# Performance work log

Hardware: AMD Instinct MI355X
Metric: run time of the kernel (lower is better)

Reference implementation:

```python
import jax, jax.numpy as jnp
import numpy as np

N_FULL, N_SUB, NNZ = 100000, 32768, 1048576
F_IN, DH, DOUT = 512, 512, 512
EPS_NORM = 1e-9   # HighOrderAggregator 'norm' bias eps
EPS_L2 = 1e-12    # F.normalize eps


def spmm(row, col, val, feat, n):
    # sparse [n,n] @ dense [n,d] via gather + segment-sum scatter
    return jax.ops.segment_sum(val[:, None] * feat[col], row, num_segments=n)


def ho_layer(row, col, val, feat, Ws, bs, scales, offsets, n):
    # HighOrderAggregator, order=1, act=relu, bias='norm', aggr='concat'
    hops = [feat, spmm(row, col, val, feat, n)]
    parts = []
    for h, W, b, s, o in zip(hops, Ws, bs, scales, offsets):
        f = jax.nn.relu(h @ W.T + b)
        mean = jnp.mean(f, axis=1, keepdims=True)
        var = jnp.var(f, axis=1, keepdims=True)  # unbiased=False, matches torch
        parts.append((f - mean) * s * jax.lax.rsqrt(var + EPS_NORM) + o)
    return jnp.concatenate(parts, axis=1)


def _xavier(k, shape):
    fan_out, fan_in = shape
    lim = float(np.sqrt(6.0 / (fan_in + fan_out)))
    return jax.random.uniform(k, shape, jnp.float32, -lim, lim)


def setup_inputs() -> dict:
    key = jax.random.key(0)
    ks = jax.random.split(key, 24)
    inp = {}
    inp['feat_full'] = jax.random.normal(ks[0], (N_FULL, F_IN), jnp.float32)
    inp['node_subgraph'] = jax.random.randint(ks[1], (N_SUB,), 0, N_FULL)
    inp['adj_row'] = jax.random.randint(ks[2], (NNZ,), 0, N_SUB)
    inp['adj_col'] = jax.random.randint(ks[3], (NNZ,), 0, N_SUB)
    inp['adj_val'] = jax.random.uniform(ks[4], (NNZ,), jnp.float32)
    # layer 1: dim_in=512 -> 512 per order, concat -> 1024
    inp['W1_0'] = _xavier(ks[5], (DH, F_IN))
    inp['W1_1'] = _xavier(ks[6], (DH, F_IN))
    inp['b1_0'] = 0.02 * jax.random.normal(ks[7], (DH,), jnp.float32)
    inp['b1_1'] = 0.02 * jax.random.normal(ks[8], (DH,), jnp.float32)
    inp['s1_0'] = 1.0 + 0.1 * jax.random.normal(ks[9], (DH,), jnp.float32)
    inp['s1_1'] = 1.0 + 0.1 * jax.random.normal(ks[10], (DH,), jnp.float32)
    inp['o1_0'] = 0.02 * jax.random.normal(ks[11], (DH,), jnp.float32)
    inp['o1_1'] = 0.02 * jax.random.normal(ks[12], (DH,), jnp.float32)
    # layer 2: dim_in=1024 -> 512 per order, concat -> 1024
    inp['W2_0'] = _xavier(ks[13], (DH, 2 * DH))
    inp['W2_1'] = _xavier(ks[14], (DH, 2 * DH))
    inp['b2_0'] = 0.02 * jax.random.normal(ks[15], (DH,), jnp.float32)
    inp['b2_1'] = 0.02 * jax.random.normal(ks[16], (DH,), jnp.float32)
    inp['s2_0'] = 1.0 + 0.1 * jax.random.normal(ks[17], (DH,), jnp.float32)
    inp['s2_1'] = 1.0 + 0.1 * jax.random.normal(ks[18], (DH,), jnp.float32)
    inp['o2_0'] = 0.02 * jax.random.normal(ks[19], (DH,), jnp.float32)
    inp['o2_1'] = 0.02 * jax.random.normal(ks[20], (DH,), jnp.float32)
    # classifier: order=0, act='I', bias='bias'
    inp['Wc'] = _xavier(ks[21], (DOUT, 2 * DH))
    inp['bc'] = 0.02 * jax.random.normal(ks[22], (DOUT,), jnp.float32)
    return inp


def reference(feat_full, node_subgraph, adj_row, adj_col, adj_val,
              W1_0, W1_1, b1_0, b1_1, s1_0, s1_1, o1_0, o1_1,
              W2_0, W2_1, b2_0, b2_1, s2_0, s2_1, o2_0, o2_1,
              Wc, bc):
    feat = feat_full[node_subgraph]                       # [N_SUB, F_IN] gather
    h = ho_layer(adj_row, adj_col, adj_val, feat,
                 (W1_0, W1_1), (b1_0, b1_1), (s1_0, s1_1), (o1_0, o1_1), N_SUB)
    h = ho_layer(adj_row, adj_col, adj_val, h,
                 (W2_0, W2_1), (b2_0, b2_1), (s2_0, s2_1), (o2_0, o2_1), N_SUB)
    nrm = jnp.linalg.norm(h, axis=1, keepdims=True)       # F.normalize p=2 dim=1
    h = h / jnp.maximum(nrm, EPS_L2)
    return h @ Wc.T + bc                                  # classifier (act='I')
```

## Files before the change

kernel.cpp:

```cpp
#include <hip/hip_runtime.h>
#include <stdint.h>

typedef unsigned short u16;
typedef unsigned int u32;

#define NSUB 32768
#define NNZ_E 1048576

using short8 = __attribute__((ext_vector_type(8))) short;
using f32x4  = __attribute__((ext_vector_type(4))) float;

__device__ __forceinline__ u16 f2b(float f) {
  u32 u = __float_as_uint(f);
  return (u16)((u + 0x7fffu + ((u >> 16) & 1u)) >> 16);
}
__device__ __forceinline__ float b2f(u16 x) {
  return __uint_as_float(((u32)x) << 16);
}

__device__ __forceinline__ void glds16(const void* g, void* l) {
  __builtin_amdgcn_global_load_lds(
      (const __attribute__((address_space(1))) u32*)g,
      (__attribute__((address_space(3))) u32*)l, 16, 0, 0);
}

__global__ __launch_bounds__(256) void cvt_bf16(const float* __restrict__ in,
                                                u16* __restrict__ out, int n4) {
  int i = blockIdx.x * 256 + threadIdx.x;
  if (i < n4) {
    float4 v = ((const float4*)in)[i];
    ushort4 o;
    o.x = f2b(v.x); o.y = f2b(v.y); o.z = f2b(v.z); o.w = f2b(v.w);
    ((ushort4*)out)[i] = o;
  }
}

__global__ __launch_bounds__(128) void gather_cast(const float* __restrict__ ff,
                                                   const int* __restrict__ idx,
                                                   u16* __restrict__ out) {
  int r = blockIdx.x, t = threadIdx.x;
  size_t src = (size_t)idx[r];
  float4 v = *(const float4*)(ff + src * 512 + t * 4);
  ushort4 o;
  o.x = f2b(v.x); o.y = f2b(v.y); o.z = f2b(v.z); o.w = f2b(v.w);
  *(ushort4*)(out + (size_t)r * 512 + t * 4) = o;
}

__global__ __launch_bounds__(256) void edge_count(const int* __restrict__ row,
                                                  int* __restrict__ cnt) {
  int i = blockIdx.x * 256 + threadIdx.x;
  atomicAdd(&cnt[row[i]], 1);
}

__global__ __launch_bounds__(1024) void scan_rows(const int* __restrict__ cnt,
                                                  int* __restrict__ off,
                                                  int* __restrict__ cursor) {
  __shared__ int part[1024];
  int t = threadIdx.x;
  int base = t * 32;
  int sum = 0;
  for (int j = 0; j < 32; ++j) sum += cnt[base + j];
  part[t] = sum;
  __syncthreads();
  for (int d = 1; d < 1024; d <<= 1) {
    int v = part[t];
    int u = (t >= d) ? part[t - d] : 0;
    __syncthreads();
    part[t] = v + u;
    __syncthreads();
  }
  int run = part[t] - sum;
  for (int j = 0; j < 32; ++j) {
    int c = cnt[base + j];
    off[base + j] = run;
    cursor[base + j] = run;
    run += c;
  }
  if (t == 1023) off[NSUB] = part[1023];
}

__global__ __launch_bounds__(256) void edge_scatter(const int* __restrict__ row,
                                                    const int* __restrict__ col,
                                                    const float* __restrict__ val,
                                                    int* __restrict__ cursor,
                                                    int2* __restrict__ cv) {
  int i = blockIdx.x * 256 + threadIdx.x;
  int r = row[i];
  int p = atomicAdd(&cursor[r], 1);
  int2 e; e.x = col[i]; e.y = __float_as_int(val[i]);
  cv[p] = e;
}

__device__ __forceinline__ void fma8(int4 u, float v, float* a) {
  u32 w;
  w = (u32)u.x; a[0] += v * __uint_as_float(w << 16); a[1] += v * __uint_as_float(w & 0xffff0000u);
  w = (u32)u.y; a[2] += v * __uint_as_float(w << 16); a[3] += v * __uint_as_float(w & 0xffff0000u);
  w = (u32)u.z; a[4] += v * __uint_as_float(w << 16); a[5] += v * __uint_as_float(w & 0xffff0000u);
  w = (u32)u.w; a[6] += v * __uint_as_float(w << 16); a[7] += v * __uint_as_float(w & 0xffff0000u);
}

template <int LDX, bool NORM>
__global__ __launch_bounds__(256) void spmm512(const int* __restrict__ off,
                                               const int2* __restrict__ cv,
                                               const u16* __restrict__ X,
                                               u16* __restrict__ Y, int ldy,
                                               const float* __restrict__ bias,
                                               const float* __restrict__ sc,
                                               const float* __restrict__ ofs) {
  const int lane = threadIdx.x & 63, wave = threadIdx.x >> 6;
  const int r = blockIdx.x * 4 + wave;
  const int s = __builtin_amdgcn_readfirstlane(off[r]);
  const int e = __builtin_amdgcn_readfirstlane(off[r + 1]);
  float a[8] = {0.f, 0.f, 0.f, 0.f, 0.f, 0.f, 0.f, 0.f};
  const u16* Xl = X + lane * 8;
  int i = s;
  for (; i + 4 <= e; i += 4) {
    int2 p0 = cv[i], p1 = cv[i + 1], p2 = cv[i + 2], p3 = cv[i + 3];
    int4 u0 = *(const int4*)(Xl + (size_t)p0.x * LDX);
    int4 u1 = *(const int4*)(Xl + (size_t)p1.x * LDX);
    int4 u2 = *(const int4*)(Xl + (size_t)p2.x * LDX);
    int4 u3 = *(const int4*)(Xl + (size_t)p3.x * LDX);
    fma8(u0, __int_as_float(p0.y), a);
    fma8(u1, __int_as_float(p1.y), a);
    fma8(u2, __int_as_float(p2.y), a);
    fma8(u3, __int_as_float(p3.y), a);
  }
  for (; i < e; ++i) {
    int2 p0 = cv[i];
    int4 u0 = *(const int4*)(Xl + (size_t)p0.x * LDX);
    fma8(u0, __int_as_float(p0.y), a);
  }
  if (NORM) {
    float4 b0 = *(const float4*)(bias + lane * 8);
    float4 b1 = *(const float4*)(bias + lane * 8 + 4);
    a[0] = fmaxf(a[0] + b0.x, 0.f); a[1] = fmaxf(a[1] + b0.y, 0.f);
    a[2] = fmaxf(a[2] + b0.z, 0.f); a[3] = fmaxf(a[3] + b0.w, 0.f);
    a[4] = fmaxf(a[4] + b1.x, 0.f); a[5] = fmaxf(a[5] + b1.y, 0.f);
    a[6] = fmaxf(a[6] + b1.z, 0.f); a[7] = fmaxf(a[7] + b1.w, 0.f);
    float sum = 0.f, sq = 0.f;
#pragma unroll
    for (int j = 0; j < 8; ++j) { sum += a[j]; sq += a[j] * a[j]; }
#pragma unroll
    for (int d = 1; d < 64; d <<= 1) {
      sum += __shfl_xor(sum, d);
      sq  += __shfl_xor(sq, d);
    }
    float mean = sum * (1.f / 512.f);
    float var = sq * (1.f / 512.f) - mean * mean;
    float rstd = rsqrtf(var + 1e-9f);
    float4 s0 = *(const float4*)(sc + lane * 8);
    float4 s1 = *(const float4*)(sc + lane * 8 + 4);
    float4 o0 = *(const float4*)(ofs + lane * 8);
    float4 o1 = *(const float4*)(ofs + lane * 8 + 4);
    int4 o;
    o.x = (int)((u32)f2b((a[0] - mean) * s0.x * rstd + o0.x) |
                ((u32)f2b((a[1] - mean) * s0.y * rstd + o0.y) << 16));
    o.y = (int)((u32)f2b((a[2] - mean) * s0.z * rstd + o0.z) |
                ((u32)f2b((a[3] - mean) * s0.w * rstd + o0.w) << 16));
    o.z = (int)((u32)f2b((a[4] - mean) * s1.x * rstd + o1.x) |
                ((u32)f2b((a[5] - mean) * s1.y * rstd + o1.y) << 16));
    o.w = (int)((u32)f2b((a[6] - mean) * s1.z * rstd + o1.z) |
                ((u32)f2b((a[7] - mean) * s1.w * rstd + o1.w) << 16));
    *(int4*)(Y + (size_t)r * ldy + lane * 8) = o;
  } else {
    int4 o;
    o.x = (int)((u32)f2b(a[0]) | ((u32)f2b(a[1]) << 16));
    o.y = (int)((u32)f2b(a[2]) | ((u32)f2b(a[3]) << 16));
    o.z = (int)((u32)f2b(a[4]) | ((u32)f2b(a[5]) << 16));
    o.w = (int)((u32)f2b(a[6]) | ((u32)f2b(a[7]) << 16));
    *(int4*)(Y + (size_t)r * ldy + lane * 8) = o;
  }
}

template <int K, int LDC, bool BIAS, bool BF16OUT>
__global__ __launch_bounds__(256) void gemm_bt(const u16* __restrict__ A,
                                               const u16* __restrict__ W,
                                               const float* __restrict__ bias,
                                               float* __restrict__ Cf,
                                               u16* __restrict__ Cb) {
  __shared__ __align__(16) u16 As[128 * 32];
  __shared__ __align__(16) u16 Bs[128 * 32];
  const int t = threadIdx.x;
  const int lane = t & 63, wave = t >> 6;
  const int wm = (wave >> 1) * 64, wn = (wave & 1) * 64;
  const int nwg = gridDim.x * gridDim.y;
  const int bid = blockIdx.x + gridDim.x * blockIdx.y;
  const int sbid = (bid % 8) * (nwg / 8) + bid / 8;
  const int bx = sbid % gridDim.x, by = sbid / gridDim.x;
  const int m0 = by * 128, n0 = bx * 128;

  f32x4 acc[4][4];
#pragma unroll
  for (int m = 0; m < 4; ++m)
#pragma unroll
    for (int n = 0; n < 4; ++n) acc[m][n] = f32x4{0.f, 0.f, 0.f, 0.f};

  const int lr = t >> 2;
  const int lc = (t & 3) * 8;
  const u16* Ag  = A + (size_t)(m0 + lr) * K + lc;
  const u16* Ag2 = Ag + (size_t)64 * K;
  const u16* Wg  = W + (size_t)(n0 + lr) * K + lc;
  const u16* Wg2 = Wg + (size_t)64 * K;
  char* asb0 = (char*)As + wave * 1024;
  char* asb1 = (char*)As + 4096 + wave * 1024;
  char* bsb0 = (char*)Bs + wave * 1024;
  char* bsb1 = (char*)Bs + 4096 + wave * 1024;
  const int fr = lane & 15, kh = lane >> 4;

  for (int kt = 0; kt < K / 32; ++kt) {
    glds16(Ag + kt * 32, asb0);
    glds16(Ag2 + kt * 32, asb1);
    glds16(Wg + kt * 32, bsb0);
    glds16(Wg2 + kt * 32, bsb1);
    __syncthreads();
    short8 af[4], bfr[4];
#pragma unroll
    for (int m = 0; m < 4; ++m)
      af[m] = *(const short8*)&As[(wm + m * 16 + fr) * 32 + kh * 8];
#pragma unroll
    for (int n = 0; n < 4; ++n)
      bfr[n] = *(const short8*)&Bs[(wn + n * 16 + fr) * 32 + kh * 8];
#pragma unroll
    for (int m = 0; m < 4; ++m)
#pragma unroll
      for (int n = 0; n < 4; ++n)
        acc[m][n] = __builtin_amdgcn_mfma_f32_16x16x32_bf16(af[m], bfr[n], acc[m][n], 0, 0, 0);
    __syncthreads();
  }

  const int crow = (lane >> 4) * 4;
  const int ccol = lane & 15;
#pragma unroll
  for (int n = 0; n < 4; ++n) {
    int col = n0 + wn + n * 16 + ccol;
    float bv = BIAS ? bias[col] : 0.f;
#pragma unroll
    for (int m = 0; m < 4; ++m) {
      int row = m0 + wm + m * 16 + crow;
#pragma unroll
      for (int q = 0; q < 4; ++q) {
        float v = acc[m][n][q] + bv;
        if (BF16OUT)
          Cb[(size_t)(row + q) * LDC + col] = f2b(v);
        else
          Cf[(size_t)(row + q) * LDC + col] = v;
      }
    }
  }
}

__global__ __launch_bounds__(128) void rownorm_b(const u16* __restrict__ F, int ldf,
                                                 const float* __restrict__ bias,
                                                 const float* __restrict__ sc,
                                                 const float* __restrict__ ofs,
                                                 u16* __restrict__ out, int col_off) {
  int r = blockIdx.x, t = threadIdx.x;
  ushort4 uv = *(const ushort4*)(F + (size_t)r * ldf + t * 4);
  float4 b4 = *(const float4*)(bias + t * 4);
  float4 v;
  v.x = fmaxf(b2f(uv.x) + b4.x, 0.f);
  v.y = fmaxf(b2f(uv.y) + b4.y, 0.f);
  v.z = fmaxf(b2f(uv.z) + b4.z, 0.f);
  v.w = fmaxf(b2f(uv.w) + b4.w, 0.f);
  float sum = v.x + v.y + v.z + v.w;
  float sq = v.x * v.x + v.y * v.y + v.z * v.z + v.w * v.w;
  for (int d = 32; d > 0; d >>= 1) {
    sum += __shfl_down(sum, d);
    sq  += __shfl_down(sq, d);
  }
  __shared__ float red[4];
  if ((t & 63) == 0) { red[(t >> 6) * 2] = sum; red[(t >> 6) * 2 + 1] = sq; }
  __syncthreads();
  float S = red[0] + red[2], Q = red[1] + red[3];
  float mean = S * (1.f / 512.f);
  float var = Q * (1.f / 512.f) - mean * mean;
  float rstd = rsqrtf(var + 1e-9f);
  float4 s4 = *(const float4*)(sc + t * 4);
  float4 o4 = *(const float4*)(ofs + t * 4);
  ushort4 o;
  o.x = f2b((v.x - mean) * s4.x * rstd + o4.x);
  o.y = f2b((v.y - mean) * s4.y * rstd + o4.y);
  o.z = f2b((v.z - mean) * s4.z * rstd + o4.z);
  o.w = f2b((v.w - mean) * s4.w * rstd + o4.w);
  *(ushort4*)(out + (size_t)r * 1024 + col_off + t * 4) = o;
}

__global__ __launch_bounds__(256) void l2norm(u16* __restrict__ H) {
  int r = blockIdx.x, t = threadIdx.x;
  uint2 u = *(const uint2*)(H + (size_t)r * 1024 + t * 4);
  float f0 = __uint_as_float(u.x << 16);
  float f1 = __uint_as_float(u.x & 0xffff0000u);
  float f2 = __uint_as_float(u.y << 16);
  float f3 = __uint_as_float(u.y & 0xffff0000u);
  float sq = f0 * f0 + f1 * f1 + f2 * f2 + f3 * f3;
  for (int d = 32; d > 0; d >>= 1) sq += __shfl_down(sq, d);
  __shared__ float red[4];
  if ((t & 63) == 0) red[t >> 6] = sq;
  __syncthreads();
  float S = red[0] + red[1] + red[2] + red[3];
  float inv = 1.f / fmaxf(sqrtf(S), 1e-12f);
  uint2 o;
  o.x = (u32)f2b(f0 * inv) | ((u32)f2b(f1 * inv) << 16);
  o.y = (u32)f2b(f2 * inv) | ((u32)f2b(f3 * inv) << 16);
  *(uint2*)(H + (size_t)r * 1024 + t * 4) = o;
}

extern "C" void kernel_launch(void* const* d_in, const int* in_sizes, int n_in,
                              void* d_out, int out_size, void* d_ws, size_t ws_size,
                              hipStream_t stream) {
  (void)in_sizes; (void)n_in; (void)out_size; (void)ws_size;
  const float* feat_full = (const float*)d_in[0];
  const int*   nodes = (const int*)d_in[1];
  const int*   arow = (const int*)d_in[2];
  const int*   acol = (const int*)d_in[3];
  const float* aval = (const float*)d_in[4];
  const float* W1_0 = (const float*)d_in[5];
  const float* W1_1 = (const float*)d_in[6];
  const float* b1_0 = (const float*)d_in[7];
  const float* b1_1 = (const float*)d_in[8];
  const float* s1_0 = (const float*)d_in[9];
  const float* s1_1 = (const float*)d_in[10];
  const float* o1_0 = (const float*)d_in[11];
  const float* o1_1 = (const float*)d_in[12];
  const float* W2_0 = (const float*)d_in[13];
  const float* W2_1 = (const float*)d_in[14];
  const float* b2_0 = (const float*)d_in[15];
  const float* b2_1 = (const float*)d_in[16];
  const float* s2_0 = (const float*)d_in[17];
  const float* s2_1 = (const float*)d_in[18];
  const float* o2_0 = (const float*)d_in[19];
  const float* o2_1 = (const float*)d_in[20];
  const float* Wc = (const float*)d_in[21];
  const float* bc = (const float*)d_in[22];
  float* out = (float*)d_out;

  const size_t MB = (size_t)1 << 20;
  char* p = (char*)d_ws;
  u16* FEAT = (u16*)p;
  u16* S1   = (u16*)(p + 32 * MB);
  u16* H1   = (u16*)(p + 64 * MB);
  u16* H2   = (u16*)(p + 128 * MB);
  u16* TMPb = (u16*)(p + 192 * MB);
  u16* TTL  = (u16*)(p + 192 * MB);
  u16* W1_0b = (u16*)(p + 256 * MB);
  u16* W1_1b = W1_0b + 512 * 512;
  u16* W2cat = W1_1b + 512 * 512;
  u16* Wcb   = W2cat + 1024 * 1024;
  int* row_off = (int*)(p + 264 * MB);
  int* cnt    = row_off + 33024;
  int* cursor = cnt + NSUB;
  int2* cv    = (int2*)(cursor + NSUB);

  hipMemsetAsync(cnt, 0, NSUB * sizeof(int), stream);

  cvt_bf16<<<(512 * 512 / 4 + 255) / 256, 256, 0, stream>>>(W1_0, W1_0b, 512 * 512 / 4);
  cvt_bf16<<<(512 * 512 / 4 + 255) / 256, 256, 0, stream>>>(W1_1, W1_1b, 512 * 512 / 4);
  cvt_bf16<<<(512 * 1024 / 4 + 255) / 256, 256, 0, stream>>>(W2_0, W2cat, 512 * 1024 / 4);
  cvt_bf16<<<(512 * 1024 / 4 + 255) / 256, 256, 0, stream>>>(W2_1, W2cat + 512 * 1024, 512 * 1024 / 4);
  cvt_bf16<<<(512 * 1024 / 4 + 255) / 256, 256, 0, stream>>>(Wc, Wcb, 512 * 1024 / 4);

  gather_cast<<<NSUB, 128, 0, stream>>>(feat_full, nodes, FEAT);

  edge_count<<<NNZ_E / 256, 256, 0, stream>>>(arow, cnt);
  scan_rows<<<1, 1024, 0, stream>>>(cnt, row_off, cursor);
  edge_scatter<<<NNZ_E / 256, 256, 0, stream>>>(arow, acol, aval, cursor, cv);

  spmm512<512, false><<<NSUB / 4, 256, 0, stream>>>(row_off, cv, FEAT, S1, 512,
                                                    nullptr, nullptr, nullptr);
  gemm_bt<512, 512, false, true><<<dim3(4, 256), 256, 0, stream>>>(FEAT, W1_0b, nullptr, nullptr, TMPb);
  rownorm_b<<<NSUB, 128, 0, stream>>>(TMPb, 512, b1_0, s1_0, o1_0, H1, 0);
  gemm_bt<512, 512, false, true><<<dim3(4, 256), 256, 0, stream>>>(S1, W1_1b, nullptr, nullptr, TMPb);
  rownorm_b<<<NSUB, 128, 0, stream>>>(TMPb, 512, b1_1, s1_1, o1_1, H1, 512);

  gemm_bt<1024, 1024, false, true><<<dim3(8, 256), 256, 0, stream>>>(H1, W2cat, nullptr, nullptr, TTL);
  rownorm_b<<<NSUB, 128, 0, stream>>>(TTL, 1024, b2_0, s2_0, o2_0, H2, 0);
  spmm512<1024, true><<<NSUB / 4, 256, 0, stream>>>(row_off, cv, TTL + 512, H2 + 512, 1024,
                                                    b2_1, s2_1, o2_1);

  l2norm<<<NSUB, 256, 0, stream>>>(H2);
  gemm_bt<1024, 512, true, false><<<dim3(4, 256), 256, 0, stream>>>(H2, Wcb, bc, out, nullptr);
}
```

Measured before the change: 725.3 us.

## Fuse GEMM with bias-ReLU-rownorm epilogue and fold L2 norm into classifier

Adds a gemm_norm kernel in which each 512-thread block computes full 512-wide output rows for 64 rows. Bias, ReLU, mean/variance and the affine norm are applied in the epilogue, so the separate rownorm passes and their bf16 intermediate buffers are no longer needed. The L2 normalize no longer rewrites H2; a light kernel computes per-row inverse norms, and the classifier GEMM scales its accumulator by them. The trade is a 64-row tile that reloads the full weight slab per block, which lowers weight reuse and may lower MFMA efficiency compared with the 128x128 tiles.

```diff
diff --git a/kernel.cpp b/kernel.cpp
--- a/kernel.cpp
+++ b/kernel.cpp
@@ -172,10 +172,128 @@
   }
 }
 
-template <int K, int LDC, bool BIAS, bool BF16OUT>
+template <int K>
+__global__ __launch_bounds__(512) void gemm_norm(const u16* __restrict__ A,
+                                                 const u16* __restrict__ W,
+                                                 const float* __restrict__ bias,
+                                                 const float* __restrict__ sc,
+                                                 const float* __restrict__ ofs,
+                                                 u16* __restrict__ out, int col_off) {
+  __shared__ __align__(16) u16 As[64 * 32];
+  __shared__ __align__(16) u16 Bs[512 * 32];
+  __shared__ float redS[8][64];
+  __shared__ float redQ[8][64];
+  __shared__ float mrs[2][64];
+  const int t = threadIdx.x;
+  const int lane = t & 63, w = t >> 6;
+  const int wn = w * 64;
+  const int m0 = blockIdx.x * 64;
+  const int fr = lane & 15, kh = lane >> 4;
+
+  f32x4 acc[4][4];
+#pragma unroll
+  for (int m = 0; m < 4; ++m)
+#pragma unroll
+    for (int n = 0; n < 4; ++n) acc[m][n] = f32x4{0.f, 0.f, 0.f, 0.f};
+
+  const int kc8 = (lane & 3) * 8;
+  const u16* Ag = A + (size_t)(m0 + w * 16 + (lane >> 2)) * K + kc8;
+  const u16* Wg = W + (size_t)(w * 64 + (lane >> 2)) * K + kc8;
+  char* asb = (char*)As + w * 1024;
+  char* bsb = (char*)Bs + w * 4096;
+
+  for (int kt = 0; kt < K / 32; ++kt) {
+    if (w < 4) glds16(Ag + kt * 32, asb);
+    glds16(Wg + kt * 32, bsb);
+    glds16(Wg + (size_t)16 * K + kt * 32, bsb + 1024);
+    glds16(Wg + (size_t)32 * K + kt * 32, bsb + 2048);
+    glds16(Wg + (size_t)48 * K + kt * 32, bsb + 3072);
+    __syncthreads();
+    short8 af[4], bfr[4];
+#pragma unroll
+    for (int m = 0; m < 4; ++m)
+      af[m] = *(const short8*)&As[(m * 16 + fr) * 32 + kh * 8];
+#pragma unroll
+    for (int n = 0; n < 4; ++n)
+      bfr[n] = *(const short8*)&Bs[(wn + n * 16 + fr) * 32 + kh * 8];
+#pragma unroll
+    for (int m = 0; m < 4; ++m)
+#pragma unroll
+      for (int n = 0; n < 4; ++n)
+        acc[m][n] = __builtin_amdgcn_mfma_f32_16x16x32_bf16(af[m], bfr[n], acc[m][n], 0, 0, 0);
+    __syncthreads();
+  }
+
+  float bv[4], sv[4], ov[4];
+#pragma unroll
+  for (int n = 0; n < 4; ++n) {
+    int cg = wn + n * 16 + fr;
+    bv[n] = bias[cg]; sv[n] = sc[cg]; ov[n] = ofs[cg];
+  }
+  float s_[4][4], q_[4][4];
+#pragma unroll
+  for (int m = 0; m < 4; ++m)
+#pragma unroll
+    for (int q = 0; q < 4; ++q) { s_[m][q] = 0.f; q_[m][q] = 0.f; }
+#pragma unroll
+  for (int m = 0; m < 4; ++m)
+#pragma unroll
+    for (int n = 0; n < 4; ++n)
+#pragma unroll
+      for (int q = 0; q < 4; ++q) {
+        float v = fmaxf(acc[m][n][q] + bv[n], 0.f);
+        acc[m][n][q] = v;
+        s_[m][q] += v; q_[m][q] += v * v;
+      }
+#pragma unroll
+  for (int d = 1; d < 16; d <<= 1)
+#pragma unroll
+    for (int m = 0; m < 4; ++m)
+#pragma unroll
+      for (int q = 0; q < 4; ++q) {
+        s_[m][q] += __shfl_xor(s_[m][q], d);
+        q_[m][q] += __shfl_xor(q_[m][q], d);
+      }
+  if (fr == 0) {
+#pragma unroll
+    for (int m = 0; m < 4; ++m)
+#pragma unroll
+      for (int q = 0; q < 4; ++q) {
+        int row = m * 16 + kh * 4 + q;
+        redS[w][row] = s_[m][q];
+        redQ[w][row] = q_[m][q];
+      }
+  }
+  __syncthreads();
+  if (t < 64) {
+    float S = 0.f, Q = 0.f;
+#pragma unroll
+    for (int w8 = 0; w8 < 8; ++w8) { S += redS[w8][t]; Q += redQ[w8][t]; }
+    float mean = S * (1.f / 512.f);
+    float var = Q * (1.f / 512.f) - mean * mean;
+    mrs[0][t] = mean;
+    mrs[1][t] = rsqrtf(var + 1e-9f);
+  }
+  __syncthreads();
+#pragma unroll
+  for (int m = 0; m < 4; ++m)
+#pragma unroll
+    for (int q = 0; q < 4; ++q) {
+      int row = m * 16 + kh * 4 + q;
+      float mean = mrs[0][row], rstd = mrs[1][row];
+#pragma unroll
+      for (int n = 0; n < 4; ++n) {
+        float v = (acc[m][n][q] - mean) * sv[n] * rstd + ov[n];
+        out[(size_t)(m0 + row) * 1024 + col_off + wn + n * 16 + fr] = f2b(v);
+      }
+    }
+}
+
+template <int K, int LDC, bool BIAS, bool BF16OUT, bool RS>
 __global__ __launch_bounds__(256) void gemm_bt(const u16* __restrict__ A,
                                                const u16* __restrict__ W,
                                                const float* __restrict__ bias,
+                                               const float* __restrict__ rs,
                                                float* __restrict__ Cf,
                                                u16* __restrict__ Cb) {
   __shared__ __align__(16) u16 As[128 * 32];
@@ -239,7 +357,9 @@
       int row = m0 + wm + m * 16 + crow;
 #pragma unroll
       for (int q = 0; q < 4; ++q) {
-        float v = acc[m][n][q] + bv;
+        float v = acc[m][n][q];
+        if (RS) v *= rs[row + q];
+        v += bv;
         if (BF16OUT)
           Cb[(size_t)(row + q) * LDC + col] = f2b(v);
         else
@@ -249,60 +369,25 @@
   }
 }
 
-__global__ __launch_bounds__(128) void rownorm_b(const u16* __restrict__ F, int ldf,
-                                                 const float* __restrict__ bias,
-                                                 const float* __restrict__ sc,
-                                                 const float* __restrict__ ofs,
-                                                 u16* __restrict__ out, int col_off) {
-  int r = blockIdx.x, t = threadIdx.x;
-  ushort4 uv = *(const ushort4*)(F + (size_t)r * ldf + t * 4);
-  float4 b4 = *(const float4*)(bias + t * 4);
-  float4 v;
-  v.x = fmaxf(b2f(uv.x) + b4.x, 0.f);
-  v.y = fmaxf(b2f(uv.y) + b4.y, 0.f);
-  v.z = fmaxf(b2f(uv.z) + b4.z, 0.f);
-  v.w = fmaxf(b2f(uv.w) + b4.w, 0.f);
-  float sum = v.x + v.y + v.z + v.w;
-  float sq = v.x * v.x + v.y * v.y + v.z * v.z + v.w * v.w;
-  for (int d = 32; d > 0; d >>= 1) {
-    sum += __shfl_down(sum, d);
-    sq  += __shfl_down(sq, d);
-  }
-  __shared__ float red[4];
-  if ((t & 63) == 0) { red[(t >> 6) * 2] = sum; red[(t >> 6) * 2 + 1] = sq; }
-  __syncthreads();
-  float S = red[0] + red[2], Q = red[1] + red[3];
-  float mean = S * (1.f / 512.f);
-  float var = Q * (1.f / 512.f) - mean * mean;
-  float rstd = rsqrtf(var + 1e-9f);
-  float4 s4 = *(const float4*)(sc + t * 4);
-  float4 o4 = *(const float4*)(ofs + t * 4);
-  ushort4 o;
-  o.x = f2b((v.x - mean) * s4.x * rstd + o4.x);
-  o.y = f2b((v.y - mean) * s4.y * rstd + o4.y);
-  o.z = f2b((v.z - mean) * s4.z * rstd + o4.z);
-  o.w = f2b((v.w - mean) * s4.w * rstd + o4.w);
-  *(ushort4*)(out + (size_t)r * 1024 + col_off + t * 4) = o;
-}
-
-__global__ __launch_bounds__(256) void l2norm(u16* __restrict__ H) {
-  int r = blockIdx.x, t = threadIdx.x;
-  uint2 u = *(const uint2*)(H + (size_t)r * 1024 + t * 4);
-  float f0 = __uint_as_float(u.x << 16);
-  float f1 = __uint_as_float(u.x & 0xffff0000u);
-  float f2 = __uint_as_float(u.y << 16);
-  float f3 = __uint_as_float(u.y & 0xffff0000u);
-  float sq = f0 * f0 + f1 * f1 + f2 * f2 + f3 * f3;
-  for (int d = 32; d > 0; d >>= 1) sq += __shfl_down(sq, d);
-  __shared__ float red[4];
-  if ((t & 63) == 0) red[t >> 6] = sq;
-  __syncthreads();
-  float S = red[0] + red[1] + red[2] + red[3];
-  float inv = 1.f / fmaxf(sqrtf(S), 1e-12f);
-  uint2 o;
-  o.x = (u32)f2b(f0 * inv) | ((u32)f2b(f1 * inv) << 16);
-  o.y = (u32)f2b(f2 * inv) | ((u32)f2b(f3 * inv) << 16);
-  *(uint2*)(H + (size_t)r * 1024 + t * 4) = o;
+__global__ __launch_bounds__(256) void l2scale(const u16* __restrict__ H,
+                                               float* __restrict__ rn) {
+  const int lane = threadIdx.x & 63, wave = threadIdx.x >> 6;
+  const int r = blockIdx.x * 4 + wave;
+  const u16* row = H + (size_t)r * 1024 + lane * 16;
+  int4 u0 = *(const int4*)row;
+  int4 u1 = *(const int4*)(row + 8);
+  float sq = 0.f;
+  const int vals[8] = {u0.x, u0.y, u0.z, u0.w, u1.x, u1.y, u1.z, u1.w};
+#pragma unroll
+  for (int j = 0; j < 8; ++j) {
+    u32 wv = (u32)vals[j];
+    float f0 = __uint_as_float(wv << 16);
+    float f1 = __uint_as_float(wv & 0xffff0000u);
+    sq += f0 * f0 + f1 * f1;
+  }
+#pragma unroll
+  for (int d = 1; d < 64; d <<= 1) sq += __shfl_xor(sq, d);
+  if (lane == 0) rn[r] = 1.f / fmaxf(sqrtf(sq), 1e-12f);
 }
 
 extern "C" void kernel_launch(void* const* d_in, const int* in_sizes, int n_in,
@@ -340,12 +425,13 @@
   u16* S1   = (u16*)(p + 32 * MB);
   u16* H1   = (u16*)(p + 64 * MB);
   u16* H2   = (u16*)(p + 128 * MB);
-  u16* TMPb = (u16*)(p + 192 * MB);
-  u16* TTL  = (u16*)(p + 192 * MB);
+  u16* G2   = (u16*)(p + 192 * MB);
+  float* RN = (float*)(p + 224 * MB);
   u16* W1_0b = (u16*)(p + 256 * MB);
   u16* W1_1b = W1_0b + 512 * 512;
-  u16* W2cat = W1_1b + 512 * 512;
-  u16* Wcb   = W2cat + 1024 * 1024;
+  u16* W2_0b = W1_1b + 512 * 512;
+  u16* W2_1b = W2_0b + 512 * 1024;
+  u16* Wcb   = W2_1b + 512 * 1024;
   int* row_off = (int*)(p + 264 * MB);
   int* cnt    = row_off + 33024;
   int* cursor = cnt + NSUB;
@@ -355,8 +441,8 @@
 
   cvt_bf16<<<(512 * 512 / 4 + 255) / 256, 256, 0, stream>>>(W1_0, W1_0b, 512 * 512 / 4);
   cvt_bf16<<<(512 * 512 / 4 + 255) / 256, 256, 0, stream>>>(W1_1, W1_1b, 512 * 512 / 4);
-  cvt_bf16<<<(512 * 1024 / 4 + 255) / 256, 256, 0, stream>>>(W2_0, W2cat, 512 * 1024 / 4);
-  cvt_bf16<<<(512 * 1024 / 4 + 255) / 256, 256, 0, stream>>>(W2_1, W2cat + 512 * 1024, 512 * 1024 / 4);
+  cvt_bf16<<<(512 * 1024 / 4 + 255) / 256, 256, 0, stream>>>(W2_0, W2_0b, 512 * 1024 / 4);
+  cvt_bf16<<<(512 * 1024 / 4 + 255) / 256, 256, 0, stream>>>(W2_1, W2_1b, 512 * 1024 / 4);
   cvt_bf16<<<(512 * 1024 / 4 + 255) / 256, 256, 0, stream>>>(Wc, Wcb, 512 * 1024 / 4);
 
   gather_cast<<<NSUB, 128, 0, stream>>>(feat_full, nodes, FEAT);
@@ -367,16 +453,16 @@
 
   spmm512<512, false><<<NSUB / 4, 256, 0, stream>>>(row_off, cv, FEAT, S1, 512,
                                                     nullptr, nullptr, nullptr);
-  gemm_bt<512, 512, false, true><<<dim3(4, 256), 256, 0, stream>>>(FEAT, W1_0b, nullptr, nullptr, TMPb);
-  rownorm_b<<<NSUB, 128, 0, stream>>>(TMPb, 512, b1_0, s1_0, o1_0, H1, 0);
-  gemm_bt<512, 512, false, true><<<dim3(4, 256), 256, 0, stream>>>(S1, W1_1b, nullptr, nullptr, TMPb);
-  rownorm_b<<<NSUB, 128, 0, stream>>>(TMPb, 512, b1_1, s1_1, o1_1, H1, 512);
-
-  gemm_bt<1024, 1024, false, true><<<dim3(8, 256), 256, 0, stream>>>(H1, W2cat, nullptr, nullptr, TTL);
-  rownorm_b<<<NSUB, 128, 0, stream>>>(TTL, 1024, b2_0, s2_0, o2_0, H2, 0);
-  spmm512<1024, true><<<NSUB / 4, 256, 0, stream>>>(row_off, cv, TTL + 512, H2 + 512, 1024,
-                                                    b2_1, s2_1, o2_1);
-
-  l2norm<<<NSUB, 256, 0, stream>>>(H2);
-  gemm_bt<1024, 512, true, false><<<dim3(4, 256), 256, 0, stream>>>(H2, Wcb, bc, out, nullptr);
-}
+  gemm_norm<512><<<NSUB / 64, 512, 0, stream>>>(FEAT, W1_0b, b1_0, s1_0, o1_0, H1, 0);
+  gemm_norm<512><<<NSUB / 64, 512, 0, stream>>>(S1, W1_1b, b1_1, s1_1, o1_1, H1, 512);
+
+  gemm_norm<1024><<<NSUB / 64, 512, 0, stream>>>(H1, W2_0b, b2_0, s2_0, o2_0, H2, 0);
+  gemm_bt<1024, 512, false, true, false><<<dim3(4, 256), 256, 0, stream>>>(
+      H1, W2_1b, nullptr, nullptr, nullptr, G2);
+  spmm512<512, true><<<NSUB / 4, 256, 0, stream>>>(row_off, cv, G2, H2 + 512, 1024,
+                                                   b2_1, s2_1, o2_1);
+
+  l2scale<<<NSUB / 4, 256, 0, stream>>>(H2, RN);
+  gemm_bt<1024, 512, true, false, true><<<dim3(4, 256), 256, 0, stream>>>(
+      H2, Wcb, bc, RN, out, nullptr);
+}
```

Result: slower. 768.0 us (+5.9%).

## Bucket CSR edges by column block; fold L2 norm into classifier GEMM epilogue

Applied to the files above, without the earlier changes.

Edges within each row are now grouped into 8 column buckets (col>>12), so SpMM gathers within a row hit nearby X rows, which is meant to improve cache locality. The count and scan work grows eightfold to 262144 counters, all scanned by a single block. The L2 normalization no longer rewrites H2 in place. A per-row inverse norm is computed instead and applied as a row scale in the classifier GEMM epilogue, saving one read-write pass over H2 in exchange for a slightly different rounding order (no bf16 rounding of the normalized values).

```diff
diff --git a/kernel.cpp b/kernel.cpp
--- a/kernel.cpp
+++ b/kernel.cpp
@@ -46,20 +46,21 @@
   *(ushort4*)(out + (size_t)r * 512 + t * 4) = o;
 }
 
-__global__ __launch_bounds__(256) void edge_count(const int* __restrict__ row,
-                                                  int* __restrict__ cnt) {
+__global__ __launch_bounds__(256) void edge_count8(const int* __restrict__ row,
+                                                   const int* __restrict__ col,
+                                                   int* __restrict__ cnt8) {
   int i = blockIdx.x * 256 + threadIdx.x;
-  atomicAdd(&cnt[row[i]], 1);
-}
-
-__global__ __launch_bounds__(1024) void scan_rows(const int* __restrict__ cnt,
-                                                  int* __restrict__ off,
-                                                  int* __restrict__ cursor) {
+  atomicAdd(&cnt8[row[i] * 8 + (col[i] >> 12)], 1);
+}
+
+__global__ __launch_bounds__(1024) void scan_rows8(const int* __restrict__ cnt8,
+                                                   int* __restrict__ off,
+                                                   int* __restrict__ cursor8) {
   __shared__ int part[1024];
   int t = threadIdx.x;
-  int base = t * 32;
+  int base = t * 256;
   int sum = 0;
-  for (int j = 0; j < 32; ++j) sum += cnt[base + j];
+  for (int j = 0; j < 256; ++j) sum += cnt8[base + j];
   part[t] = sum;
   __syncthreads();
   for (int d = 1; d < 1024; d <<= 1) {
@@ -70,24 +71,25 @@
     __syncthreads();
   }
   int run = part[t] - sum;
-  for (int j = 0; j < 32; ++j) {
-    int c = cnt[base + j];
-    off[base + j] = run;
-    cursor[base + j] = run;
+  for (int j = 0; j < 256; ++j) {
+    int idx = base + j;
+    int c = cnt8[idx];
+    cursor8[idx] = run;
+    if ((idx & 7) == 0) off[idx >> 3] = run;
     run += c;
   }
-  if (t == 1023) off[NSUB] = part[1023];
-}
-
-__global__ __launch_bounds__(256) void edge_scatter(const int* __restrict__ row,
-                                                    const int* __restrict__ col,
-                                                    const float* __restrict__ val,
-                                                    int* __restrict__ cursor,
-                                                    int2* __restrict__ cv) {
+  if (t == 1023) off[NSUB] = run;
+}
+
+__global__ __launch_bounds__(256) void edge_scatter8(const int* __restrict__ row,
+                                                     const int* __restrict__ col,
+                                                     const float* __restrict__ val,
+                                                     int* __restrict__ cursor8,
+                                                     int2* __restrict__ cv) {
   int i = blockIdx.x * 256 + threadIdx.x;
-  int r = row[i];
-  int p = atomicAdd(&cursor[r], 1);
-  int2 e; e.x = col[i]; e.y = __float_as_int(val[i]);
+  int c = col[i];
+  int p = atomicAdd(&cursor8[row[i] * 8 + (c >> 12)], 1);
+  int2 e; e.x = c; e.y = __float_as_int(val[i]);
   cv[p] = e;
 }
 
@@ -172,10 +174,11 @@
   }
 }
 
-template <int K, int LDC, bool BIAS, bool BF16OUT>
+template <int K, int LDC, bool BIAS, bool BF16OUT, bool RS>
 __global__ __launch_bounds__(256) void gemm_bt(const u16* __restrict__ A,
                                                const u16* __restrict__ W,
                                                const float* __restrict__ bias,
+                                               const float* __restrict__ rs,
                                                float* __restrict__ Cf,
                                                u16* __restrict__ Cb) {
   __shared__ __align__(16) u16 As[128 * 32];
@@ -239,7 +242,9 @@
       int row = m0 + wm + m * 16 + crow;
 #pragma unroll
       for (int q = 0; q < 4; ++q) {
-        float v = acc[m][n][q] + bv;
+        float v = acc[m][n][q];
+        if (RS) v *= rs[row + q];
+        v += bv;
         if (BF16OUT)
           Cb[(size_t)(row + q) * LDC + col] = f2b(v);
         else
@@ -285,24 +290,25 @@
   *(ushort4*)(out + (size_t)r * 1024 + col_off + t * 4) = o;
 }
 
-__global__ __launch_bounds__(256) void l2norm(u16* __restrict__ H) {
-  int r = blockIdx.x, t = threadIdx.x;
-  uint2 u = *(const uint2*)(H + (size_t)r * 1024 + t * 4);
-  float f0 = __uint_as_float(u.x << 16);
-  float f1 = __uint_as_float(u.x & 0xffff0000u);
-  float f2 = __uint_as_float(u.y << 16);
-  float f3 = __uint_as_float(u.y & 0xffff0000u);
-  float sq = f0 * f0 + f1 * f1 + f2 * f2 + f3 * f3;
-  for (int d = 32; d > 0; d >>= 1) sq += __shfl_down(sq, d);
-  __shared__ float red[4];
-  if ((t & 63) == 0) red[t >> 6] = sq;
-  __syncthreads();
-  float S = red[0] + red[1] + red[2] + red[3];
-  float inv = 1.f / fmaxf(sqrtf(S), 1e-12f);
-  uint2 o;
-  o.x = (u32)f2b(f0 * inv) | ((u32)f2b(f1 * inv) << 16);
-  o.y = (u32)f2b(f2 * inv) | ((u32)f2b(f3 * inv) << 16);
-  *(uint2*)(H + (size_t)r * 1024 + t * 4) = o;
+__global__ __launch_bounds__(256) void l2scale(const u16* __restrict__ H,
+                                               float* __restrict__ rn) {
+  const int lane = threadIdx.x & 63, wave = threadIdx.x >> 6;
+  const int r = blockIdx.x * 4 + wave;
+  const u16* row = H + (size_t)r * 1024 + lane * 16;
+  int4 u0 = *(const int4*)row;
+  int4 u1 = *(const int4*)(row + 8);
+  float sq = 0.f;
+  const int vals[8] = {u0.x, u0.y, u0.z, u0.w, u1.x, u1.y, u1.z, u1.w};
+#pragma unroll
+  for (int j = 0; j < 8; ++j) {
+    u32 wv = (u32)vals[j];
+    float f0 = __uint_as_float(wv << 16);
+    float f1 = __uint_as_float(wv & 0xffff0000u);
+    sq += f0 * f0 + f1 * f1;
+  }
+#pragma unroll
+  for (int d = 1; d < 64; d <<= 1) sq += __shfl_xor(sq, d);
+  if (lane == 0) rn[r] = 1.f / fmaxf(sqrtf(sq), 1e-12f);
 }
 
 extern "C" void kernel_launch(void* const* d_in, const int* in_sizes, int n_in,
@@ -346,12 +352,13 @@
   u16* W1_1b = W1_0b + 512 * 512;
   u16* W2cat = W1_1b + 512 * 512;
   u16* Wcb   = W2cat + 1024 * 1024;
-  int* row_off = (int*)(p + 264 * MB);
-  int* cnt    = row_off + 33024;
-  int* cursor = cnt + NSUB;
-  int2* cv    = (int2*)(cursor + NSUB);
-
-  hipMemsetAsync(cnt, 0, NSUB * sizeof(int), stream);
+  int* row_off = (int*)(p + 260 * MB);
+  int* cnt8    = (int*)(p + 261 * MB);
+  int* cursor8 = (int*)(p + 262 * MB);
+  float* RN    = (float*)(p + 263 * MB);
+  int2* cv     = (int2*)(p + 264 * MB);
+
+  hipMemsetAsync(cnt8, 0, NSUB * 8 * sizeof(int), stream);
 
   cvt_bf16<<<(512 * 512 / 4 + 255) / 256, 256, 0, stream>>>(W1_0, W1_0b, 512 * 512 / 4);
   cvt_bf16<<<(512 * 512 / 4 + 255) / 256, 256, 0, stream>>>(W1_1, W1_1b, 512 * 512 / 4);
@@ -361,22 +368,26 @@
 
   gather_cast<<<NSUB, 128, 0, stream>>>(feat_full, nodes, FEAT);
 
-  edge_count<<<NNZ_E / 256, 256, 0, stream>>>(arow, cnt);
-  scan_rows<<<1, 1024, 0, stream>>>(cnt, row_off, cursor);
-  edge_scatter<<<NNZ_E / 256, 256, 0, stream>>>(arow, acol, aval, cursor, cv);
+  edge_count8<<<NNZ_E / 256, 256, 0, stream>>>(arow, acol, cnt8);
+  scan_rows8<<<1, 1024, 0, stream>>>(cnt8, row_off, cursor8);
+  edge_scatter8<<<NNZ_E / 256, 256, 0, stream>>>(arow, acol, aval, cursor8, cv);
 
   spmm512<512, false><<<NSUB / 4, 256, 0, stream>>>(row_off, cv, FEAT, S1, 512,
                                                     nullptr, nullptr, nullptr);
-  gemm_bt<512, 512, false, true><<<dim3(4, 256), 256, 0, stream>>>(FEAT, W1_0b, nullptr, nullptr, TMPb);
+  gemm_bt<512, 512, false, true, false><<<dim3(4, 256), 256, 0, stream>>>(
+      FEAT, W1_0b, nullptr, nullptr, nullptr, TMPb);
   rownorm_b<<<NSUB, 128, 0, stream>>>(TMPb, 512, b1_0, s1_0, o1_0, H1, 0);
-  gemm_bt<512, 512, false, true><<<dim3(4, 256), 256, 0, stream>>>(S1, W1_1b, nullptr, nullptr, TMPb);
+  gemm_bt<512, 512, false, true, false><<<dim3(4, 256), 256, 0, stream>>>(
+      S1, W1_1b, nullptr, nullptr, nullptr, TMPb);
   rownorm_b<<<NSUB, 128, 0, stream>>>(TMPb, 512, b1_1, s1_1, o1_1, H1, 512);
 
-  gemm_bt<1024, 1024, false, true><<<dim3(8, 256), 256, 0, stream>>>(H1, W2cat, nullptr, nullptr, TTL);
+  gemm_bt<1024, 1024, false, true, false><<<dim3(8, 256), 256, 0, stream>>>(
+      H1, W2cat, nullptr, nullptr, nullptr, TTL);
   rownorm_b<<<NSUB, 128, 0, stream>>>(TTL, 1024, b2_0, s2_0, o2_0, H2, 0);
   spmm512<1024, true><<<NSUB / 4, 256, 0, stream>>>(row_off, cv, TTL + 512, H2 + 512, 1024,
                                                     b2_1, s2_1, o2_1);
 
-  l2norm<<<NSUB, 256, 0, stream>>>(H2);
-  gemm_bt<1024, 512, true, false><<<dim3(4, 256), 256, 0, stream>>>(H2, Wcb, bc, out, nullptr);
-}
+  l2scale<<<NSUB / 4, 256, 0, stream>>>(H2, RN);
+  gemm_bt<1024, 512, true, false, true><<<dim3(4, 256), 256, 0, stream>>>(
+      H2, Wcb, bc, RN, out, nullptr);
+}
```

Result: slower. 894.2 us (+23.3%).
